# Kernel tuning notes

Measured on AMD Instinct MI355X. Metric: run time of the kernel, lower is better.

The kernel has to match this reference:

```python
import jax, jax.numpy as jnp
import numpy as np

D_MODEL = 1024
H = 16
D_K = D_MODEL // H
D_FF = 4096
EPS = 1e-6


def setup_inputs() -> dict:
    key = jax.random.key(0)
    ks = jax.random.split(key, 12)
    s = 0.02
    inp = {
        "x": jax.random.normal(ks[0], (2, 2048, D_MODEL), jnp.float32),
        # attention projection weights stored [in, out] (y = x @ W + b)
        "Wq": jax.random.normal(ks[1], (D_MODEL, D_MODEL), jnp.float32) * s,
        "bq": jnp.zeros((D_MODEL,), jnp.float32),
        "Wk": jax.random.normal(ks[2], (D_MODEL, D_MODEL), jnp.float32) * s,
        "bk": jnp.zeros((D_MODEL,), jnp.float32),
        "Wv": jax.random.normal(ks[3], (D_MODEL, D_MODEL), jnp.float32) * s,
        "bv": jnp.zeros((D_MODEL,), jnp.float32),
        "Wo": jax.random.normal(ks[4], (D_MODEL, D_MODEL), jnp.float32) * s,
        "bo": jnp.zeros((D_MODEL,), jnp.float32),
        # FFN
        "W1": jax.random.normal(ks[5], (D_MODEL, D_FF), jnp.float32) * s,
        "b1": jnp.zeros((D_FF,), jnp.float32),
        "W2": jax.random.normal(ks[6], (D_FF, D_MODEL), jnp.float32) * s,
        "b2": jnp.zeros((D_MODEL,), jnp.float32),
        # scalar LayerNorm params (as in the source: nn.Parameter(torch.ones(1)))
        "ln1_alpha": jnp.ones((1,), jnp.float32),
        "ln1_beta": jnp.ones((1,), jnp.float32),
        "ln2_alpha": jnp.ones((1,), jnp.float32),
        "ln2_beta": jnp.ones((1,), jnp.float32),
    }
    return inp


def _layernorm(x, alpha, beta):
    # Faithful to source: unbiased std (ddof=1), divide by (std + eps)
    mean = jnp.mean(x, axis=-1, keepdims=True)
    var = jnp.var(x, axis=-1, keepdims=True, ddof=1)
    std = jnp.sqrt(var)
    return alpha * (x - mean) / (std + EPS) + beta


def _mha(x, Wq, bq, Wk, bk, Wv, bv, Wo, bo):
    B, S, _ = x.shape
    q = (x @ Wq + bq).reshape(B, S, H, D_K).transpose(0, 2, 1, 3)
    k = (x @ Wk + bk).reshape(B, S, H, D_K).transpose(0, 2, 1, 3)
    v = (x @ Wv + bv).reshape(B, S, H, D_K).transpose(0, 2, 1, 3)
    # NOTE: source has no 1/sqrt(d_k) scaling
    scores = jnp.einsum('bhqd,bhkd->bhqk', q, k)
    attn = jax.nn.softmax(scores, axis=-1)
    out = jnp.einsum('bhqk,bhkd->bhqd', attn, v)
    out = out.transpose(0, 2, 1, 3).reshape(B, S, D_MODEL)
    return out @ Wo + bo


def reference(x, Wq, bq, Wk, bk, Wv, bv, Wo, bo, W1, b1, W2, b2,
              ln1_alpha, ln1_beta, ln2_alpha, ln2_beta):
    # pre-norm residual 1: self-attention (dropout=0, eval mode)
    h = x + _mha(_layernorm(x, ln1_alpha, ln1_beta), Wq, bq, Wk, bk, Wv, bv, Wo, bo)
    # pre-norm residual 2: FFN
    n = _layernorm(h, ln2_alpha, ln2_beta)
    ffn = jax.nn.relu(n @ W1 + b1) @ W2 + b2
    return h + ffn
```

## Files before the change

kernel.cpp:

```cpp
#include <hip/hip_runtime.h>

#define DMODEL 1024
#define DFF    4096
#define SEQ    2048
#define NTOK   4096
#define QKVN   3072
#define LOG2E  1.4426950408889634f

typedef unsigned short u16;
typedef short s8v __attribute__((ext_vector_type(8)));
typedef float f4v __attribute__((ext_vector_type(4)));

__device__ __forceinline__ u16 f2bf(float f) {
  union { float f; unsigned u; } c; c.f = f;
  unsigned r = c.u + 0x7fffu + ((c.u >> 16) & 1u);
  return (u16)(r >> 16);
}
__device__ __forceinline__ float u2f(unsigned u) {
  union { unsigned u; float f; } c; c.u = u; return c.f;
}

__device__ __forceinline__ unsigned cvt_pk_bf16(float lo, float hi) {
  unsigned r;
  asm("v_cvt_pk_bf16_f32 %0, %1, %2" : "=v"(r) : "v"(lo), "v"(hi));
  return r;
}
__device__ __forceinline__ void pl32swap(unsigned& x, unsigned& y) {
  asm("v_permlane32_swap_b32 %0, %1" : "+v"(x), "+v"(y));
}
__device__ __forceinline__ void pl16swap(unsigned& x, unsigned& y) {
  asm("v_permlane16_swap_b32 %0, %1" : "+v"(x), "+v"(y));
}

typedef const __attribute__((address_space(1))) unsigned GAS;
typedef __attribute__((address_space(3))) unsigned LAS;
__device__ __forceinline__ void gl2lds16(const void* g, void* l) {
  __builtin_amdgcn_global_load_lds((GAS*)g, (LAS*)l, 16, 0, 0);
}

__device__ __forceinline__ void tr32(const float* __restrict__ W, u16* __restrict__ Wt,
                                     int K, int N, int bx, int by, float (*sh)[33],
                                     float scale) {
  int n0 = bx * 32, k0 = by * 32;
  int tx = threadIdx.x & 31, ty = threadIdx.x >> 5;
#pragma unroll
  for (int r = ty; r < 32; r += 8) sh[r][tx] = W[(size_t)(k0 + r) * N + n0 + tx];
  __syncthreads();
#pragma unroll
  for (int r = ty; r < 32; r += 8) Wt[(size_t)(n0 + r) * K + k0 + tx] = f2bf(sh[tx][r] * scale);
}

__global__ __launch_bounds__(256)
void prep(const float* __restrict__ Wq, const float* __restrict__ Wk,
          const float* __restrict__ Wv, const float* __restrict__ Wo,
          const float* __restrict__ W1, const float* __restrict__ W2,
          const float* __restrict__ bq, const float* __restrict__ bk,
          const float* __restrict__ bv,
          u16* __restrict__ wqkv_t, u16* __restrict__ wo_t,
          u16* __restrict__ w1_t, u16* __restrict__ w2_t, float* __restrict__ bqkv) {
  __shared__ float sh[32][33];
  int b = blockIdx.x;
  if (b < 1024) {
    tr32(Wq, wqkv_t, 1024, 1024, b & 31, b >> 5, sh, LOG2E);
  } else if (b < 2048) {
    b -= 1024; tr32(Wk, wqkv_t + (1u << 20), 1024, 1024, b & 31, b >> 5, sh, 1.0f);
  } else if (b < 3072) {
    b -= 2048; tr32(Wv, wqkv_t + (2u << 20), 1024, 1024, b & 31, b >> 5, sh, 1.0f);
  } else if (b < 4096) {
    b -= 3072; tr32(Wo, wo_t, 1024, 1024, b & 31, b >> 5, sh, 1.0f);
  } else if (b < 8192) {
    b -= 4096; tr32(W1, w1_t, 1024, 4096, b & 127, b >> 7, sh, 1.0f);
  } else if (b < 12288) {
    b -= 8192; tr32(W2, w2_t, 4096, 1024, b & 31, b >> 5, sh, 1.0f);
  } else {
    int t = (b - 12288) * 256 + threadIdx.x;
    float v = (t < 1024) ? bq[t] * LOG2E : (t < 2048 ? bk[t - 1024] : bv[t - 2048]);
    bqkv[t] = v;
  }
}

__global__ __launch_bounds__(256)
void ln_bf16(const float* __restrict__ X, u16* __restrict__ Y,
             const float* __restrict__ a_p, const float* __restrict__ b_p) {
  int row = blockIdx.x;
  const float4* xr = (const float4*)(X + (size_t)row * DMODEL);
  float4 v = xr[threadIdx.x];
  float s  = v.x + v.y + v.z + v.w;
  float ss = v.x * v.x + v.y * v.y + v.z * v.z + v.w * v.w;
#pragma unroll
  for (int m = 32; m >= 1; m >>= 1) { s += __shfl_xor(s, m, 64); ss += __shfl_xor(ss, m, 64); }
  __shared__ float red[8];
  int wid = threadIdx.x >> 6, lane = threadIdx.x & 63;
  if (lane == 0) { red[wid] = s; red[4 + wid] = ss; }
  __syncthreads();
  s  = red[0] + red[1] + red[2] + red[3];
  ss = red[4] + red[5] + red[6] + red[7];
  float mean = s * (1.0f / 1024.0f);
  float var  = fmaxf((ss - s * mean) * (1.0f / 1023.0f), 0.0f);
  float k    = a_p[0] / (sqrtf(var) + 1e-6f);
  float beta = b_p[0];
  ushort4 o;
  o.x = f2bf((v.x - mean) * k + beta);
  o.y = f2bf((v.y - mean) * k + beta);
  o.z = f2bf((v.z - mean) * k + beta);
  o.w = f2bf((v.w - mean) * k + beta);
  ((ushort4*)(Y + (size_t)row * DMODEL))[threadIdx.x] = o;
}

template <int RELU, int RESID, int OUT_BF16, int ATOMIC>
__global__ __launch_bounds__(256, 3)
void gemm_bt(const u16* __restrict__ A, const u16* __restrict__ Bt,
             const float* __restrict__ bias, const float* __restrict__ resid,
             void* __restrict__ Cout, int M, int N, int K) {
  __shared__ __align__(16) u16 As[128 * 64];
  __shared__ __align__(16) u16 Bs[128 * 64];
  const int lane = threadIdx.x & 63, wid = threadIdx.x >> 6;
  const int llo = lane & 15, lhi = lane >> 4;

  const int nwg = gridDim.x * gridDim.y;
  int lin = blockIdx.y * gridDim.x + blockIdx.x;
  if ((nwg & 7) == 0) lin = (lin & 7) * (nwg >> 3) + (lin >> 3);
  const int m0 = (lin / gridDim.x) * 128, n0 = (lin % gridDim.x) * 128;

  const int wm = wid & 1, wn = wid >> 1;
  const int r8 = lane >> 3;
  const int c8 = ((lane & 7) ^ r8) * 8;

  f4v acc[4][4];
  const f4v fz = {0.f, 0.f, 0.f, 0.f};
#pragma unroll
  for (int i = 0; i < 4; ++i)
#pragma unroll
    for (int j = 0; j < 4; ++j) acc[i][j] = fz;

  const u16* Ag = A  + (size_t)(m0 + r8) * K + c8;
  const u16* Bg = Bt + (size_t)(n0 + r8) * K + c8;

  const int Kp = ATOMIC ? (K / gridDim.z) : K;
  const int kbeg = ATOMIC ? blockIdx.z * Kp : 0;
  const int kend = kbeg + Kp;

  for (int kt = kbeg; kt < kend; kt += 64) {
#pragma unroll
    for (int c = 0; c < 4; ++c) {
      int ch = wid * 4 + c;
      gl2lds16(Ag + (size_t)(ch * 8) * K + kt, As + ch * 512);
      gl2lds16(Bg + (size_t)(ch * 8) * K + kt, Bs + ch * 512);
    }
    __syncthreads();
#pragma unroll
    for (int ks = 0; ks < 2; ++ks) {
      const int so = ((ks * 4 + lhi) ^ (llo & 7)) * 8;
      s8v a[4], b[4];
#pragma unroll
      for (int i = 0; i < 4; ++i)
        a[i] = *(const s8v*)&As[(wm * 64 + i * 16 + llo) * 64 + so];
#pragma unroll
      for (int j = 0; j < 4; ++j)
        b[j] = *(const s8v*)&Bs[(wn * 64 + j * 16 + llo) * 64 + so];
#pragma unroll
      for (int i = 0; i < 4; ++i)
#pragma unroll
        for (int j = 0; j < 4; ++j)
          acc[i][j] = __builtin_amdgcn_mfma_f32_16x16x32_bf16(a[i], b[j], acc[i][j], 0, 0, 0);
    }
    __syncthreads();
  }
#pragma unroll
  for (int j = 0; j < 4; ++j) {
    int col = n0 + wn * 64 + j * 16 + llo;
    float bv = bias[col];
#pragma unroll
    for (int i = 0; i < 4; ++i) {
      int r0 = m0 + wm * 64 + i * 16 + lhi * 4;
#pragma unroll
      for (int r = 0; r < 4; ++r) {
        size_t idx = (size_t)(r0 + r) * N + col;
        float v = acc[i][j][r];
        if (ATOMIC) {
          if (blockIdx.z == 0) {
            v += bv;
            if (RESID) v += resid[idx];
          }
          atomicAdd(&((float*)Cout)[idx], v);
        } else {
          v += bv;
          if (RESID) v += resid[idx];
          if (RELU) v = fmaxf(v, 0.0f);
          if (OUT_BF16) ((u16*)Cout)[idx] = f2bf(v);
          else          ((float*)Cout)[idx] = v;
        }
      }
    }
  }
}

template <int RELU, int OUT_BF16>
__global__ __launch_bounds__(512, 2)
void gemm256(const u16* __restrict__ A, const u16* __restrict__ Bt,
             const float* __restrict__ bias, void* __restrict__ Cout,
             int M, int N, int K) {
  __shared__ __align__(16) u16 As[2][256 * 64];
  __shared__ __align__(16) u16 Bs[2][256 * 64];
  const int lane = threadIdx.x & 63, wid = threadIdx.x >> 6;
  const int llo = lane & 15, lhi = lane >> 4;
  const int wr = wid >> 2, wc = wid & 3;

  const int nwg = gridDim.x * gridDim.y;
  int lin = blockIdx.y * gridDim.x + blockIdx.x;
  if ((nwg & 7) == 0) lin = (lin & 7) * (nwg >> 3) + (lin >> 3);
  const int m0 = (lin / gridDim.x) * 256, n0 = (lin % gridDim.x) * 256;

  const int r8 = lane >> 3;
  const int c8 = ((lane & 7) ^ r8) * 8;

  f4v acc[8][4];
  const f4v fz = {0.f, 0.f, 0.f, 0.f};
#pragma unroll
  for (int i = 0; i < 8; ++i)
#pragma unroll
    for (int j = 0; j < 4; ++j) acc[i][j] = fz;

  const u16* Ag = A  + (size_t)(m0 + r8) * K + c8;
  const u16* Bg = Bt + (size_t)(n0 + r8) * K + c8;
  const int nk = K >> 6;

  auto stage = [&](int buf, int kt) {
#pragma unroll
    for (int c = 0; c < 4; ++c) {
      int ch = wid * 4 + c;
      gl2lds16(Ag + (size_t)(ch * 8) * K + kt, As[buf] + ch * 512);
      gl2lds16(Bg + (size_t)(ch * 8) * K + kt, Bs[buf] + ch * 512);
    }
  };

  stage(0, 0);
  __syncthreads();
  int cur = 0;
  for (int t = 0; t < nk; ++t) {
    if (t + 1 < nk) stage(cur ^ 1, (t + 1) * 64);
#pragma unroll
    for (int ks = 0; ks < 2; ++ks) {
      const int so = ((ks * 4 + lhi) ^ (llo & 7)) * 8;
      s8v b[4];
#pragma unroll
      for (int j = 0; j < 4; ++j)
        b[j] = *(const s8v*)&Bs[cur][(wc * 64 + j * 16 + llo) * 64 + so];
#pragma unroll
      for (int i = 0; i < 8; ++i) {
        s8v a = *(const s8v*)&As[cur][(wr * 128 + i * 16 + llo) * 64 + so];
#pragma unroll
        for (int j = 0; j < 4; ++j)
          acc[i][j] = __builtin_amdgcn_mfma_f32_16x16x32_bf16(a, b[j], acc[i][j], 0, 0, 0);
      }
    }
    __syncthreads();
    cur ^= 1;
  }
#pragma unroll
  for (int j = 0; j < 4; ++j) {
    int col = n0 + wc * 64 + j * 16 + llo;
    float bv = bias[col];
#pragma unroll
    for (int i = 0; i < 8; ++i) {
      int r0 = m0 + wr * 128 + i * 16 + lhi * 4;
#pragma unroll
      for (int r = 0; r < 4; ++r) {
        size_t idx = (size_t)(r0 + r) * N + col;
        float v = acc[i][j][r] + bv;
        if (RELU) v = fmaxf(v, 0.0f);
        if (OUT_BF16) ((u16*)Cout)[idx] = f2bf(v);
        else          ((float*)Cout)[idx] = v;
      }
    }
  }
}

__global__ __launch_bounds__(256, 3)
void flash_attn(const u16* __restrict__ QKV, u16* __restrict__ Pacc,
                float* __restrict__ Pml) {
  __shared__ __align__(16) u16 smem[16896];
  u16* Ks = smem;
  u16* Vt = smem + 8192;

  const int tid = threadIdx.x;
  const int lane = tid & 63, wid = tid >> 6;
  const int llo = lane & 15, lhi = lane >> 4;
  int lin = blockIdx.y * 16 + blockIdx.x;
  lin = (lin & 7) * 64 + (lin >> 3);
  const int qt = lin & 15, bh = lin >> 4, z = blockIdx.z;
  const int b = bh >> 4, h = bh & 15;
  const int LDM = QKVN;
  const size_t base = (size_t)b * SEQ * LDM + h * 64;
  const u16* Qb = QKV + base + (size_t)qt * 128 * LDM;
  const u16* Kb = QKV + base + 1024;
  const u16* Vb = QKV + base + 2048;
  const int r8 = lane >> 3;
  const int c8 = ((lane & 7) ^ r8) * 8;

#pragma unroll
  for (int c = 0; c < 4; ++c) {
    int ch = wid * 4 + c;
    gl2lds16(Qb + (size_t)(ch * 8 + r8) * LDM + c8, Ks + ch * 512);
  }
  __syncthreads();
  s8v qf[2][2];
#pragma unroll
  for (int mb = 0; mb < 2; ++mb)
#pragma unroll
    for (int ks = 0; ks < 2; ++ks)
      qf[mb][ks] = *(const s8v*)&Ks[(wid * 32 + mb * 16 + llo) * 64 +
                                    (((ks * 4 + lhi) ^ (llo & 7)) * 8)];
  __syncthreads();

  f4v accO[2][4];
  float l_run[2] = {0.f, 0.f};
  const f4v fz = {0.f, 0.f, 0.f, 0.f};
#pragma unroll
  for (int mb = 0; mb < 2; ++mb)
#pragma unroll
    for (int db = 0; db < 4; ++db) accO[mb][db] = fz;

  for (int kt = z * 8; kt < z * 8 + 8; ++kt) {
#pragma unroll
    for (int c = 0; c < 4; ++c) {
      int ch = wid * 4 + c;
      gl2lds16(Kb + (size_t)(kt * 128 + ch * 8 + r8) * LDM + c8, Ks + ch * 512);
    }
#pragma unroll
    for (int it = 0; it < 2; ++it) {
      int o  = wid + it * 4;
      int k2 = lane * 2;
      const u16* vp = Vb + (size_t)(kt * 128 + k2) * LDM + o * 8;
      s8v v0 = *(const s8v*)vp;
      s8v v1 = *(const s8v*)(vp + LDM);
      const u16* e0 = (const u16*)&v0;
      const u16* e1 = (const u16*)&v1;
#pragma unroll
      for (int j = 0; j < 8; ++j) {
        unsigned pk = (unsigned)e0[j] | ((unsigned)e1[j] << 16);
        *(unsigned*)&Vt[(o * 8 + j) * 136 + k2] = pk;
      }
    }
    __syncthreads();

    s8v pa[2][4];
#pragma unroll
    for (int ksb = 0; ksb < 4; ++ksb) {
      f4v sA[2], sB[2];
#pragma unroll
      for (int mb = 0; mb < 2; ++mb) { sA[mb] = fz; sB[mb] = fz; }
#pragma unroll
      for (int ks = 0; ks < 2; ++ks) {
        const int so = ((ks * 4 + lhi) ^ (llo & 7)) * 8;
        s8v kfA = *(const s8v*)&Ks[((ksb * 2 + 0) * 16 + llo) * 64 + so];
        s8v kfB = *(const s8v*)&Ks[((ksb * 2 + 1) * 16 + llo) * 64 + so];
#pragma unroll
        for (int mb = 0; mb < 2; ++mb) {
          sA[mb] = __builtin_amdgcn_mfma_f32_16x16x32_bf16(kfA, qf[mb][ks], sA[mb], 0, 0, 0);
          sB[mb] = __builtin_amdgcn_mfma_f32_16x16x32_bf16(kfB, qf[mb][ks], sB[mb], 0, 0, 0);
        }
      }
#pragma unroll
      for (int mb = 0; mb < 2; ++mb) {
        float pA0 = __builtin_amdgcn_exp2f(sA[mb][0]);
        float pA1 = __builtin_amdgcn_exp2f(sA[mb][1]);
        float pA2 = __builtin_amdgcn_exp2f(sA[mb][2]);
        float pA3 = __builtin_amdgcn_exp2f(sA[mb][3]);
        float pB0 = __builtin_amdgcn_exp2f(sB[mb][0]);
        float pB1 = __builtin_amdgcn_exp2f(sB[mb][1]);
        float pB2 = __builtin_amdgcn_exp2f(sB[mb][2]);
        float pB3 = __builtin_amdgcn_exp2f(sB[mb][3]);
        l_run[mb] += ((pA0 + pA1) + (pA2 + pA3)) + ((pB0 + pB1) + (pB2 + pB3));
        unsigned a0 = cvt_pk_bf16(pA0, pA1), a1 = cvt_pk_bf16(pA2, pA3);
        unsigned b0 = cvt_pk_bf16(pB0, pB1), b1 = cvt_pk_bf16(pB2, pB3);
        pl32swap(a0, b0); pl16swap(a0, b0);
        pl32swap(a1, b1); pl16swap(a1, b1);
        union { unsigned u[4]; s8v v; } pk;
        pk.u[0] = a0; pk.u[1] = a1; pk.u[2] = b0; pk.u[3] = b1;
        pa[mb][ksb] = pk.v;
      }
    }

#pragma unroll
    for (int ks = 0; ks < 4; ++ks) {
      s8v vb2[4];
#pragma unroll
      for (int db = 0; db < 4; ++db)
        vb2[db] = *(const s8v*)&Vt[(db * 16 + llo) * 136 + ks * 32 + lhi * 8];
#pragma unroll
      for (int mb = 0; mb < 2; ++mb)
#pragma unroll
        for (int db = 0; db < 4; ++db)
          accO[mb][db] = __builtin_amdgcn_mfma_f32_16x16x32_bf16(pa[mb][ks], vb2[db], accO[mb][db], 0, 0, 0);
    }
    __syncthreads();
  }

#pragma unroll
  for (int mb = 0; mb < 2; ++mb) {
    l_run[mb] += __shfl_xor(l_run[mb], 16, 64);
    l_run[mb] += __shfl_xor(l_run[mb], 32, 64);
  }
#pragma unroll
  for (int mb = 0; mb < 2; ++mb) {
    int row0 = qt * 128 + wid * 32 + mb * 16;
    size_t ibase = (size_t)(z * 32 + bh) * SEQ + row0;
    if (lane < 16) Pml[ibase + lane] = l_run[mb];
#pragma unroll
    for (int r = 0; r < 4; ++r) {
      size_t irow = ibase + lhi * 4 + r;
#pragma unroll
      for (int db = 0; db < 4; ++db)
        Pacc[irow * 64 + db * 16 + llo] = f2bf(accO[mb][db][r]);
    }
  }
}

__global__ __launch_bounds__(256)
void attn_combine(const u16* __restrict__ Pacc, const float* __restrict__ Pml,
                  u16* __restrict__ ctx) {
  int g = blockIdx.x * 256 + threadIdx.x;
  int d2 = g & 31;
  int row = (g >> 5) & (SEQ - 1);
  int bh = g >> 16;
  int b = bh >> 4, h = bh & 15;
  size_t i0 = (size_t)bh * SEQ + row;
  size_t i1 = (size_t)(32 + bh) * SEQ + row;
  float inv = 1.0f / (Pml[i0] + Pml[i1]);
  unsigned pa = ((const unsigned*)Pacc)[i0 * 32 + d2];
  unsigned pb = ((const unsigned*)Pacc)[i1 * 32 + d2];
  float lo = u2f(pa << 16) + u2f(pb << 16);
  float hi = u2f(pa & 0xffff0000u) + u2f(pb & 0xffff0000u);
  unsigned o = (unsigned)f2bf(lo * inv) | ((unsigned)f2bf(hi * inv) << 16);
  ((unsigned*)ctx)[(size_t)(b * SEQ + row) * (DMODEL / 2) + h * 32 + d2] = o;
}

extern "C" void kernel_launch(void* const* d_in, const int* in_sizes, int n_in,
                              void* d_out, int out_size, void* d_ws, size_t ws_size,
                              hipStream_t stream) {
  const float* x   = (const float*)d_in[0];
  const float* Wq  = (const float*)d_in[1];  const float* bq = (const float*)d_in[2];
  const float* Wk  = (const float*)d_in[3];  const float* bk = (const float*)d_in[4];
  const float* Wv  = (const float*)d_in[5];  const float* bv = (const float*)d_in[6];
  const float* Wo  = (const float*)d_in[7];  const float* bo = (const float*)d_in[8];
  const float* W1  = (const float*)d_in[9];  const float* b1 = (const float*)d_in[10];
  const float* W2  = (const float*)d_in[11]; const float* b2 = (const float*)d_in[12];
  const float* l1a = (const float*)d_in[13]; const float* l1b = (const float*)d_in[14];
  const float* l2a = (const float*)d_in[15]; const float* l2b = (const float*)d_in[16];

  char* ws = (char*)d_ws;
  const size_t MB = 1u << 20;
  u16*   wqkv_t = (u16*)(ws + 0);
  u16*   wo_t   = (u16*)(ws + 6 * MB);
  u16*   w1_t   = (u16*)(ws + 8 * MB);
  u16*   w2_t   = (u16*)(ws + 16 * MB);
  float* bqkv   = (float*)(ws + 24 * MB);
  u16*   xn1    = (u16*)(ws + 25 * MB);
  u16*   qkv    = (u16*)(ws + 33 * MB);
  u16*   ctx    = (u16*)(ws + 57 * MB);
  float* hbuf   = (float*)(ws + 65 * MB);
  u16*   Pacc   = (u16*)(ws + 81 * MB);
  float* Pml    = (float*)(ws + 97 * MB);
  u16*   n2     = (u16*)(ws + 81 * MB);
  u16*   mid    = (u16*)(ws + 25 * MB);

  dim3 blk(256);

  hipMemsetAsync(d_out, 0, (size_t)NTOK * DMODEL * 4, stream);
  hipMemsetAsync(hbuf, 0, (size_t)NTOK * DMODEL * 4, stream);

  prep<<<dim3(12300), blk, 0, stream>>>(Wq, Wk, Wv, Wo, W1, W2, bq, bk, bv,
                                        wqkv_t, wo_t, w1_t, w2_t, bqkv);

  ln_bf16<<<NTOK, blk, 0, stream>>>(x, xn1, l1a, l1b);

  gemm256<0, 1><<<dim3(12, 16), dim3(512), 0, stream>>>(xn1, wqkv_t, bqkv, qkv,
                                                        NTOK, QKVN, DMODEL);

  flash_attn<<<dim3(16, 32, 2), blk, 0, stream>>>(qkv, Pacc, Pml);
  attn_combine<<<dim3(8192), blk, 0, stream>>>(Pacc, Pml, ctx);

  gemm_bt<0, 1, 0, 1><<<dim3(8, 32, 2), blk, 0, stream>>>(ctx, wo_t, bo, x, hbuf,
                                                          NTOK, DMODEL, DMODEL);

  ln_bf16<<<NTOK, blk, 0, stream>>>(hbuf, n2, l2a, l2b);

  gemm256<1, 1><<<dim3(16, 16), dim3(512), 0, stream>>>(n2, w1_t, b1, mid,
                                                        NTOK, DFF, DMODEL);

  gemm_bt<0, 1, 0, 1><<<dim3(8, 32, 2), blk, 0, stream>>>(mid, w2_t, b2, hbuf, (float*)d_out,
                                                          NTOK, DMODEL, DFF);
}
```

Measured before the change: 394.4 us.

## Double-buffer gemm_bt LDS and prefetch two k-tiles ahead with explicit vmcnt waits

Adds double-buffered LDS to gemm_bt and changes both GEMM kernels to issue global-to-LDS loads two tiles ahead. Explicit s_waitcnt vmcnt(8) and raw s_barrier calls replace __syncthreads, so the loads of the next tile stay in flight while the current one is consumed. MFMA sections are wrapped in s_setprio to favour matrix issue. gemm_bt now uses twice the LDS and its occupancy hint drops from 3 to 2 workgroups per CU. The hand-written vmcnt counts rely on the exact number of outstanding loads.

```diff
diff --git a/kernel.cpp b/kernel.cpp
--- a/kernel.cpp
+++ b/kernel.cpp
@@ -37,6 +37,14 @@
 __device__ __forceinline__ void gl2lds16(const void* g, void* l) {
   __builtin_amdgcn_global_load_lds((GAS*)g, (LAS*)l, 16, 0, 0);
 }
+
+__device__ __forceinline__ void bar() {
+  asm volatile("" ::: "memory");
+  __builtin_amdgcn_s_barrier();
+  asm volatile("" ::: "memory");
+}
+#define WAITVM8() asm volatile("s_waitcnt vmcnt(8)" ::: "memory")
+#define WAITVM0() asm volatile("s_waitcnt vmcnt(0)" ::: "memory")
 
 __device__ __forceinline__ void tr32(const float* __restrict__ W, u16* __restrict__ Wt,
                                      int K, int N, int bx, int by, float (*sh)[33],
@@ -108,12 +116,12 @@
 }
 
 template <int RELU, int RESID, int OUT_BF16, int ATOMIC>
-__global__ __launch_bounds__(256, 3)
+__global__ __launch_bounds__(256, 2)
 void gemm_bt(const u16* __restrict__ A, const u16* __restrict__ Bt,
              const float* __restrict__ bias, const float* __restrict__ resid,
              void* __restrict__ Cout, int M, int N, int K) {
-  __shared__ __align__(16) u16 As[128 * 64];
-  __shared__ __align__(16) u16 Bs[128 * 64];
+  __shared__ __align__(16) u16 As[2][128 * 64];
+  __shared__ __align__(16) u16 Bs[2][128 * 64];
   const int lane = threadIdx.x & 63, wid = threadIdx.x >> 6;
   const int llo = lane & 15, lhi = lane >> 4;
 
@@ -138,33 +146,50 @@
 
   const int Kp = ATOMIC ? (K / gridDim.z) : K;
   const int kbeg = ATOMIC ? blockIdx.z * Kp : 0;
-  const int kend = kbeg + Kp;
-
-  for (int kt = kbeg; kt < kend; kt += 64) {
+  const int nk = Kp >> 6;
+
+  auto stage = [&](int buf, int kt) {
 #pragma unroll
     for (int c = 0; c < 4; ++c) {
       int ch = wid * 4 + c;
-      gl2lds16(Ag + (size_t)(ch * 8) * K + kt, As + ch * 512);
-      gl2lds16(Bg + (size_t)(ch * 8) * K + kt, Bs + ch * 512);
-    }
-    __syncthreads();
+      gl2lds16(Ag + (size_t)(ch * 8) * K + kt, As[buf] + ch * 512);
+      gl2lds16(Bg + (size_t)(ch * 8) * K + kt, Bs[buf] + ch * 512);
+    }
+  };
+
+  stage(0, kbeg);
+  if (nk > 1) { stage(1, kbeg + 64); WAITVM8(); }
+  else        { WAITVM0(); }
+  bar();
+  int cur = 0;
+  for (int t = 0; t < nk; ++t) {
 #pragma unroll
     for (int ks = 0; ks < 2; ++ks) {
       const int so = ((ks * 4 + lhi) ^ (llo & 7)) * 8;
       s8v a[4], b[4];
 #pragma unroll
       for (int i = 0; i < 4; ++i)
-        a[i] = *(const s8v*)&As[(wm * 64 + i * 16 + llo) * 64 + so];
+        a[i] = *(const s8v*)&As[cur][(wm * 64 + i * 16 + llo) * 64 + so];
 #pragma unroll
       for (int j = 0; j < 4; ++j)
-        b[j] = *(const s8v*)&Bs[(wn * 64 + j * 16 + llo) * 64 + so];
+        b[j] = *(const s8v*)&Bs[cur][(wn * 64 + j * 16 + llo) * 64 + so];
+      __builtin_amdgcn_s_setprio(1);
 #pragma unroll
       for (int i = 0; i < 4; ++i)
 #pragma unroll
         for (int j = 0; j < 4; ++j)
           acc[i][j] = __builtin_amdgcn_mfma_f32_16x16x32_bf16(a[i], b[j], acc[i][j], 0, 0, 0);
-    }
-    __syncthreads();
+      __builtin_amdgcn_s_setprio(0);
+    }
+    bar();
+    if (t + 2 < nk) {
+      stage(cur, kbeg + (t + 2) * 64);
+      WAITVM8();
+    } else if (t + 1 < nk) {
+      WAITVM0();
+    }
+    bar();
+    cur ^= 1;
   }
 #pragma unroll
   for (int j = 0; j < 4; ++j) {
@@ -235,10 +260,11 @@
   };
 
   stage(0, 0);
-  __syncthreads();
+  if (nk > 1) { stage(1, 64); WAITVM8(); }
+  else        { WAITVM0(); }
+  bar();
   int cur = 0;
   for (int t = 0; t < nk; ++t) {
-    if (t + 1 < nk) stage(cur ^ 1, (t + 1) * 64);
 #pragma unroll
     for (int ks = 0; ks < 2; ++ks) {
       const int so = ((ks * 4 + lhi) ^ (llo & 7)) * 8;
@@ -246,6 +272,7 @@
 #pragma unroll
       for (int j = 0; j < 4; ++j)
         b[j] = *(const s8v*)&Bs[cur][(wc * 64 + j * 16 + llo) * 64 + so];
+      __builtin_amdgcn_s_setprio(1);
 #pragma unroll
       for (int i = 0; i < 8; ++i) {
         s8v a = *(const s8v*)&As[cur][(wr * 128 + i * 16 + llo) * 64 + so];
@@ -253,8 +280,16 @@
         for (int j = 0; j < 4; ++j)
           acc[i][j] = __builtin_amdgcn_mfma_f32_16x16x32_bf16(a, b[j], acc[i][j], 0, 0, 0);
       }
-    }
-    __syncthreads();
+      __builtin_amdgcn_s_setprio(0);
+    }
+    bar();
+    if (t + 2 < nk) {
+      stage(cur, (t + 2) * 64);
+      WAITVM8();
+    } else if (t + 1 < nk) {
+      WAITVM0();
+    }
+    bar();
     cur ^= 1;
   }
 #pragma unroll
```

Result: no change. 398.2 us (+1.0%).

## Replace atomic split-K reduction with partial buffers and fused combine

Applied to the files above, without the earlier changes.

The two split-K output GEMMs no longer zero their outputs with memsets and accumulate through global atomicAdd. Instead, the z=0 slice stores its result directly and the z=1 slice writes a separate partial buffer. For the Wo projection, a new ln2_comb kernel adds the two partials while computing LayerNorm 2. For W2, a new add2 kernel merges them. Workspace buffers are re-laid out so the partials reuse dead regions; the cost is an extra 16 MB pass for the final add and more workspace traffic.

```diff
diff --git a/kernel.cpp b/kernel.cpp
--- a/kernel.cpp
+++ b/kernel.cpp
@@ -107,11 +107,53 @@
   ((ushort4*)(Y + (size_t)row * DMODEL))[threadIdx.x] = o;
 }
 
-template <int RELU, int RESID, int OUT_BF16, int ATOMIC>
+__global__ __launch_bounds__(256)
+void ln2_comb(float* __restrict__ H, const float* __restrict__ P1,
+              u16* __restrict__ Y, const float* __restrict__ a_p,
+              const float* __restrict__ b_p) {
+  int row = blockIdx.x;
+  float4* hr = (float4*)(H + (size_t)row * DMODEL);
+  float4 v = hr[threadIdx.x];
+  float4 p = ((const float4*)(P1 + (size_t)row * DMODEL))[threadIdx.x];
+  v.x += p.x; v.y += p.y; v.z += p.z; v.w += p.w;
+  hr[threadIdx.x] = v;
+  float s  = v.x + v.y + v.z + v.w;
+  float ss = v.x * v.x + v.y * v.y + v.z * v.z + v.w * v.w;
+#pragma unroll
+  for (int m = 32; m >= 1; m >>= 1) { s += __shfl_xor(s, m, 64); ss += __shfl_xor(ss, m, 64); }
+  __shared__ float red[8];
+  int wid = threadIdx.x >> 6, lane = threadIdx.x & 63;
+  if (lane == 0) { red[wid] = s; red[4 + wid] = ss; }
+  __syncthreads();
+  s  = red[0] + red[1] + red[2] + red[3];
+  ss = red[4] + red[5] + red[6] + red[7];
+  float mean = s * (1.0f / 1024.0f);
+  float var  = fmaxf((ss - s * mean) * (1.0f / 1023.0f), 0.0f);
+  float k    = a_p[0] / (sqrtf(var) + 1e-6f);
+  float beta = b_p[0];
+  ushort4 o;
+  o.x = f2bf((v.x - mean) * k + beta);
+  o.y = f2bf((v.y - mean) * k + beta);
+  o.z = f2bf((v.z - mean) * k + beta);
+  o.w = f2bf((v.w - mean) * k + beta);
+  ((ushort4*)(Y + (size_t)row * DMODEL))[threadIdx.x] = o;
+}
+
+__global__ __launch_bounds__(256)
+void add2(float* __restrict__ D, const float* __restrict__ P) {
+  size_t g = (size_t)blockIdx.x * 256 + threadIdx.x;
+  float4 a = ((float4*)D)[g];
+  float4 b = ((const float4*)P)[g];
+  a.x += b.x; a.y += b.y; a.z += b.z; a.w += b.w;
+  ((float4*)D)[g] = a;
+}
+
+template <int RELU, int RESID, int OUT_BF16, int SPLIT>
 __global__ __launch_bounds__(256, 3)
 void gemm_bt(const u16* __restrict__ A, const u16* __restrict__ Bt,
              const float* __restrict__ bias, const float* __restrict__ resid,
-             void* __restrict__ Cout, int M, int N, int K) {
+             void* __restrict__ Cout, float* __restrict__ Cpart,
+             int M, int N, int K) {
   __shared__ __align__(16) u16 As[128 * 64];
   __shared__ __align__(16) u16 Bs[128 * 64];
   const int lane = threadIdx.x & 63, wid = threadIdx.x >> 6;
@@ -136,8 +178,8 @@
   const u16* Ag = A  + (size_t)(m0 + r8) * K + c8;
   const u16* Bg = Bt + (size_t)(n0 + r8) * K + c8;
 
-  const int Kp = ATOMIC ? (K / gridDim.z) : K;
-  const int kbeg = ATOMIC ? blockIdx.z * Kp : 0;
+  const int Kp = SPLIT ? (K / gridDim.z) : K;
+  const int kbeg = SPLIT ? blockIdx.z * Kp : 0;
   const int kend = kbeg + Kp;
 
   for (int kt = kbeg; kt < kend; kt += 64) {
@@ -177,12 +219,14 @@
       for (int r = 0; r < 4; ++r) {
         size_t idx = (size_t)(r0 + r) * N + col;
         float v = acc[i][j][r];
-        if (ATOMIC) {
+        if (SPLIT) {
           if (blockIdx.z == 0) {
             v += bv;
             if (RESID) v += resid[idx];
+            ((float*)Cout)[idx] = v;
+          } else {
+            Cpart[idx] = v;
           }
-          atomicAdd(&((float*)Cout)[idx], v);
         } else {
           v += bv;
           if (RESID) v += resid[idx];
@@ -458,17 +502,16 @@
   float* bqkv   = (float*)(ws + 24 * MB);
   u16*   xn1    = (u16*)(ws + 25 * MB);
   u16*   qkv    = (u16*)(ws + 33 * MB);
-  u16*   ctx    = (u16*)(ws + 57 * MB);
-  float* hbuf   = (float*)(ws + 65 * MB);
-  u16*   Pacc   = (u16*)(ws + 81 * MB);
-  float* Pml    = (float*)(ws + 97 * MB);
-  u16*   n2     = (u16*)(ws + 81 * MB);
+  u16*   Pacc   = (u16*)(ws + 57 * MB);
+  float* Pml    = (float*)(ws + 73 * MB);
+  u16*   ctx    = (u16*)(ws + 73 * MB + MB / 2);
+  float* hgm    = (float*)(ws + 57 * MB);
+  float* po1    = (float*)(ws + 25 * MB);
+  u16*   n2     = (u16*)(ws + 73 * MB + MB / 2);
   u16*   mid    = (u16*)(ws + 25 * MB);
+  float* pf     = (float*)(ws + 73 * MB + MB / 2);
 
   dim3 blk(256);
-
-  hipMemsetAsync(d_out, 0, (size_t)NTOK * DMODEL * 4, stream);
-  hipMemsetAsync(hbuf, 0, (size_t)NTOK * DMODEL * 4, stream);
 
   prep<<<dim3(12300), blk, 0, stream>>>(Wq, Wk, Wv, Wo, W1, W2, bq, bk, bv,
                                         wqkv_t, wo_t, w1_t, w2_t, bqkv);
@@ -481,14 +524,17 @@
   flash_attn<<<dim3(16, 32, 2), blk, 0, stream>>>(qkv, Pacc, Pml);
   attn_combine<<<dim3(8192), blk, 0, stream>>>(Pacc, Pml, ctx);
 
-  gemm_bt<0, 1, 0, 1><<<dim3(8, 32, 2), blk, 0, stream>>>(ctx, wo_t, bo, x, hbuf,
+  gemm_bt<0, 1, 0, 1><<<dim3(8, 32, 2), blk, 0, stream>>>(ctx, wo_t, bo, x, hgm, po1,
                                                           NTOK, DMODEL, DMODEL);
 
-  ln_bf16<<<NTOK, blk, 0, stream>>>(hbuf, n2, l2a, l2b);
+  ln2_comb<<<NTOK, blk, 0, stream>>>(hgm, po1, n2, l2a, l2b);
 
   gemm256<1, 1><<<dim3(16, 16), dim3(512), 0, stream>>>(n2, w1_t, b1, mid,
                                                         NTOK, DFF, DMODEL);
 
-  gemm_bt<0, 1, 0, 1><<<dim3(8, 32, 2), blk, 0, stream>>>(mid, w2_t, b2, hbuf, (float*)d_out,
+  gemm_bt<0, 1, 0, 1><<<dim3(8, 32, 2), blk, 0, stream>>>(mid, w2_t, b2, hgm,
+                                                          (float*)d_out, pf,
                                                           NTOK, DMODEL, DFF);
-}
+
+  add2<<<dim3(4096), blk, 0, stream>>>((float*)d_out, pf);
+}
```

Result: faster. 358.4 us (-9.1%).
